# Optimization experiments

Measured on AMD Instinct MI355X. Metric: run time of the kernel, lower is better.

Reference implementation:

```python
import jax, jax.numpy as jnp
import numpy as np

B, N, L, H = 8, 64, 256, 768
E = 2 * H            # 1536, concat(subj, obj)
NH = 12              # attention heads
HD = E // NH         # 128 head dim
HL = 1024            # LSTM hidden
C = 42               # num classes
SCALE = 0.02         # param scale for numerical sanity


def setup_inputs() -> dict:
    key = jax.random.key(0)
    ks = jax.random.split(key, 19)
    rn = lambda k, s: jax.random.normal(k, s, jnp.float32) * SCALE
    return {
        "hidden": jax.random.normal(ks[0], (B, N, L, H), jnp.float32),
        "entity_pair_inds": jax.random.randint(ks[1], (B, N, 2), 0, L),
        "Wkey": jax.random.uniform(ks[2], (E, E), jnp.float32) * SCALE,
        "Wque": jax.random.uniform(ks[3], (E, E), jnp.float32) * SCALE,
        "Wval": jax.random.uniform(ks[4], (E, E), jnp.float32) * SCALE,
        "in_proj_w": rn(ks[5], (3 * E, E)),
        "in_proj_b": rn(ks[6], (3 * E,)),
        "out_proj_w": rn(ks[7], (E, E)),
        "out_proj_b": rn(ks[8], (E,)),
        "Wih_f": rn(ks[9], (4 * HL, E)),
        "Whh_f": rn(ks[10], (4 * HL, HL)),
        "bih_f": rn(ks[11], (4 * HL,)),
        "bhh_f": rn(ks[12], (4 * HL,)),
        "Wih_b": rn(ks[13], (4 * HL, E)),
        "Whh_b": rn(ks[14], (4 * HL, HL)),
        "bih_b": rn(ks[15], (4 * HL,)),
        "bhh_b": rn(ks[16], (4 * HL,)),
        "out_w": rn(ks[17], (C, 2 * HL)),
        "out_b": rn(ks[18], (C,)),
    }


def _mha(q_in, k_in, v_in, in_proj_w, in_proj_b, out_proj_w, out_proj_b):
    # torch nn.MultiheadAttention, batch_first
    Wq, Wk, Wv = jnp.split(in_proj_w, 3, axis=0)
    bq, bk, bv = jnp.split(in_proj_b, 3, axis=0)
    b, n, _ = q_in.shape
    q = (q_in @ Wq.T + bq).reshape(b, n, NH, HD)
    k = (k_in @ Wk.T + bk).reshape(b, n, NH, HD)
    v = (v_in @ Wv.T + bv).reshape(b, n, NH, HD)
    scores = jnp.einsum("bnhd,bmhd->bhnm", q, k) / np.sqrt(HD).astype(np.float32)
    attn = jax.nn.softmax(scores, axis=-1)
    o = jnp.einsum("bhnm,bmhd->bnhd", attn, v).reshape(b, n, E)
    return o @ out_proj_w.T + out_proj_b


def _lstm_dir(x, Wih, Whh, bih, bhh):
    # single-direction LSTM over an unbatched sequence x: (T, E)
    def step(carry, xt):
        h, c = carry
        g = xt @ Wih.T + bih + h @ Whh.T + bhh  # (4*HL,)
        i, f, gg, o = jnp.split(g, 4)
        i, f, o = jax.nn.sigmoid(i), jax.nn.sigmoid(f), jax.nn.sigmoid(o)
        c = f * c + i * jnp.tanh(gg)
        h = o * jnp.tanh(c)
        return (h, c), h
    init = (jnp.zeros(HL, x.dtype), jnp.zeros(HL, x.dtype))
    _, hs = jax.lax.scan(step, init, x)
    return hs  # (T, HL)


def reference(hidden, entity_pair_inds, Wkey, Wque, Wval, in_proj_w, in_proj_b,
              out_proj_w, out_proj_b, Wih_f, Whh_f, bih_f, bhh_f,
              Wih_b, Whh_b, bih_b, bhh_b, out_w, out_b):
    # vectorized entity-pair gather: (B, N, 2) indices into token axis L
    idx = entity_pair_inds[:, :, :, None]                      # (B,N,2,1)
    pair = jnp.take_along_axis(hidden, idx, axis=2)            # (B,N,2,H)
    cat = pair.reshape(B, N, 2 * H)                            # (B,N,1536) = [subj; obj]
    keys = cat @ Wkey
    queries = cat @ Wque
    values = cat @ Wval
    # original calls attn(keys, queries, values) -> query=keys, key=queries, value=values
    attn_out = _mha(keys, queries, values, in_proj_w, in_proj_b, out_proj_w, out_proj_b)
    avg = jnp.sum(attn_out * cat, axis=1) / N                  # (B, E)
    # dropout is identity in eval mode
    # torch LSTM treats 2D input as unbatched sequence of length B
    hf = _lstm_dir(avg, Wih_f, Whh_f, bih_f, bhh_f)            # (B, HL)
    hb = _lstm_dir(avg[::-1], Wih_b, Whh_b, bih_b, bhh_b)[::-1]
    lstm_out = jnp.concatenate([hf, hb], axis=-1)              # (B, 2*HL)
    logits = lstm_out @ out_w.T + out_b                        # (B, C)
    return jax.nn.softmax(logits, axis=1)
```

## Files before the change

### kernel.cpp

```cpp
#include <hip/hip_runtime.h>
#include <hip/hip_bf16.h>
#include <cstdint>


typedef __attribute__((ext_vector_type(8))) short short8_t;
typedef __attribute__((ext_vector_type(4))) float f32x4_t;

__device__ __forceinline__ uint4 pack8(float4 a, float4 b) {
  union { uint4 u; __hip_bfloat16 h[8]; } pk;
  pk.h[0] = __float2bfloat16(a.x); pk.h[1] = __float2bfloat16(a.y);
  pk.h[2] = __float2bfloat16(a.z); pk.h[3] = __float2bfloat16(a.w);
  pk.h[4] = __float2bfloat16(b.x); pk.h[5] = __float2bfloat16(b.y);
  pk.h[6] = __float2bfloat16(b.z); pk.h[7] = __float2bfloat16(b.w);
  return pk.u;
}

__global__ __launch_bounds__(256) void prep_all_kernel(
    const float* __restrict__ hidden, const int* __restrict__ inds,
    const float* __restrict__ Wkey, const float* __restrict__ Wque, const float* __restrict__ Wval,
    float* __restrict__ cat, __hip_bfloat16* __restrict__ cat16,
    __hip_bfloat16* __restrict__ Wt16, float* __restrict__ avg0) {
  const int bid = blockIdx.x, tid = threadIdx.x;
  if (bid < 512) {
    if (bid < 48) avg0[bid * 256 + tid] = 0.f;
    int bn = bid;
    int i0 = inds[bn * 2 + 0], i1 = inds[bn * 2 + 1];
    const float* r0 = hidden + ((size_t)bn * 256 + i0) * 768;
    const float* r1 = hidden + ((size_t)bn * 256 + i1) * 768;
    float* c = cat + (size_t)bn * 1536;
    __hip_bfloat16* c16 = cat16 + (size_t)bn * 1536;
    for (int i = tid; i < 768; i += 256) {
      float a = r0[i], b = r1[i];
      c[i] = a; c[768 + i] = b;
      c16[i] = __float2bfloat16(a); c16[768 + i] = __float2bfloat16(b);
    }
  } else {
    int b2 = bid - 512;
    int z = b2 / 576, rem = b2 % 576, by = rem / 24, bx = rem % 24;
    const float* W = z == 0 ? Wkey : (z == 1 ? Wque : Wval);
    __hip_bfloat16* O = Wt16 + (size_t)z * 1536 * 1536;
    __shared__ float tile[64][65];
    int n0 = bx * 64, k0 = by * 64;
    int r = tid >> 2, q = tid & 3;
#pragma unroll
    for (int j = 0; j < 4; ++j) {
      float4 v = *(const float4*)(W + (size_t)(k0 + r) * 1536 + n0 + q * 16 + j * 4);
      tile[r][q * 16 + j * 4 + 0] = v.x; tile[r][q * 16 + j * 4 + 1] = v.y;
      tile[r][q * 16 + j * 4 + 2] = v.z; tile[r][q * 16 + j * 4 + 3] = v.w;
    }
    __syncthreads();
    union { uint4 u[2]; __hip_bfloat16 h[16]; } pk;
#pragma unroll
    for (int i = 0; i < 16; ++i) pk.h[i] = __float2bfloat16(tile[q * 16 + i][r]);
    __hip_bfloat16* dst = O + (size_t)(n0 + r) * 1536 + k0 + q * 16;
    *(uint4*)dst = pk.u[0];
    *(uint4*)(dst + 8) = pk.u[1];
  }
}

template <int CMODE, bool BIAS, int TAIL>
__global__ __launch_bounds__(256) void mfma_gemm(
    const __hip_bfloat16* __restrict__ A, long As,
    const __hip_bfloat16* __restrict__ Bm, long Bs,
    const float* __restrict__ bias, long biasS,
    void* __restrict__ Cp, long Cs,
    const float* __restrict__ catp, float* __restrict__ avgp,
    const float* __restrict__ tail_src_f, const float* __restrict__ tail_src_b,
    __hip_bfloat16* __restrict__ tail_dst) {
  constexpr int K = 1536, N = 1536;
  const int bid = blockIdx.x, t = threadIdx.x;
  if (TAIL == 1 && bid >= 1152) {
    int tb = bid - 1152;
#pragma unroll
    for (int c = 0; c < 4; ++c) {
      int i = tb * 1024 + c * 256 + t;
      float4 a = ((const float4*)tail_src_f)[2 * i], b = ((const float4*)tail_src_f)[2 * i + 1];
      *(uint4*)(tail_dst + (size_t)i * 8) = pack8(a, b);
    }
    return;
  }
  if (TAIL == 2 && bid >= 1152) {
    int tb = bid - 1152;
#pragma unroll
    for (int c = 0; c < 4; ++c) {
      int id = tb * 1024 + c * 256 + t;
      int lane = id & 63, half = (id >> 6) & 1, row = (id >> 7) & 4095, d = id >> 19;
      const float* W = d ? tail_src_b : tail_src_f;
      const float* srcp = W + (size_t)row * 1024 + half * 512 + lane;
      union { uint4 u; __hip_bfloat16 h[8]; } pk;
#pragma unroll
      for (int e = 0; e < 8; ++e) pk.h[e] = __float2bfloat16(srcp[e * 64]);
      *(uint4*)(tail_dst + (size_t)id * 8) = pk.u;
    }
    return;
  }
  const int L = bid % 384, z = bid / 384;
  A += (size_t)z * As; Bm += (size_t)z * Bs;
  if (BIAS) bias += (size_t)z * biasS;
  __shared__ __align__(16) short Abuf[32 * 64];
  __shared__ __align__(16) short Bbuf[64 * 64];
  const int bxs = (L & 7) + 8 * ((L >> 3) % 3);
  const int bys = (L >> 3) / 3;
  const int i0 = bys * 32, j0 = bxs * 64;
  const int lane = t & 63, wave = t >> 6;
  f32x4_t acc[2] = {};

  const int rA = t >> 3, qA = t & 7;
  const char* Ag = (const char*)(A + (size_t)(i0 + rA) * K) + qA * 16;
  char* const Asw = (char*)Abuf + ((rA * 128 + qA * 16) ^ ((rA & 7) << 4));
  const int rB0 = t >> 3, qB0 = t & 7;
  const int tb1 = t + 256, rB1 = tb1 >> 3, qB1 = tb1 & 7;
  const char* Bg0 = (const char*)(Bm + (size_t)(j0 + rB0) * K) + qB0 * 16;
  const char* Bg1 = (const char*)(Bm + (size_t)(j0 + rB1) * K) + qB1 * 16;
  char* const Bsw0 = (char*)Bbuf + ((rB0 * 128 + qB0 * 16) ^ ((rB0 & 7) << 4));
  char* const Bsw1 = (char*)Bbuf + ((rB1 * 128 + qB1 * 16) ^ ((rB1 & 7) << 4));

  for (int kb = 0; kb < K * 2; kb += 128) {
    uint4 a0 = *(const uint4*)(Ag + kb);
    uint4 b0 = *(const uint4*)(Bg0 + kb);
    uint4 b1 = *(const uint4*)(Bg1 + kb);
    __syncthreads();
    *(uint4*)Asw = a0;
    *(uint4*)Bsw0 = b0; *(uint4*)Bsw1 = b1;
    __syncthreads();
#pragma unroll
    for (int ks = 0; ks < 2; ++ks) {
      short8_t af[2], bf;
#pragma unroll
      for (int mi = 0; mi < 2; ++mi) {
        int rr = mi * 16 + (lane & 15);
        int off = (rr * 128 + ks * 64 + (lane >> 4) * 16) ^ ((rr & 7) << 4);
        af[mi] = *(const short8_t*)((const char*)Abuf + off);
      }
      {
        int rr = wave * 16 + (lane & 15);
        int off = (rr * 128 + ks * 64 + (lane >> 4) * 16) ^ ((rr & 7) << 4);
        bf = *(const short8_t*)((const char*)Bbuf + off);
      }
#pragma unroll
      for (int mi = 0; mi < 2; ++mi)
        acc[mi] = __builtin_amdgcn_mfma_f32_16x16x32_bf16(af[mi], bf, acc[mi], 0, 0, 0);
    }
  }
  const int col = j0 + wave * 16 + (lane & 15);
  if (CMODE == 2) {
    const int b = bys >> 1;
    float bv = bias[col];
    float p = 0.f;
#pragma unroll
    for (int mi = 0; mi < 2; ++mi) {
      int rbase = i0 + mi * 16 + (lane >> 4) * 4;
#pragma unroll
      for (int r = 0; r < 4; ++r)
        p += (acc[mi][r] + bv) * catp[(size_t)(rbase + r) * 1536 + col];
    }
    p += __shfl_xor(p, 16);
    p += __shfl_xor(p, 32);
    if (lane < 16) atomicAdd(&avgp[(size_t)b * 1536 + col], p * (1.0f / 64.0f));
  } else {
    float bv = BIAS ? bias[col] : 0.f;
#pragma unroll
    for (int mi = 0; mi < 2; ++mi) {
      int r0 = i0 + mi * 16 + (lane >> 4) * 4;
#pragma unroll
      for (int r = 0; r < 4; ++r) {
        float val = acc[mi][r] + bv;
        if (CMODE == 1)
          ((__hip_bfloat16*)Cp)[(size_t)z * Cs + (size_t)(r0 + r) * N + col] = __float2bfloat16(val);
        else
          ((float*)Cp)[(size_t)z * Cs + (size_t)(r0 + r) * N + col] = val;
      }
    }
  }
}

__global__ __launch_bounds__(256) void attn2_kernel(
    const __hip_bfloat16* __restrict__ qkv, __hip_bfloat16* __restrict__ o,
    const float* __restrict__ opw, __hip_bfloat16* __restrict__ outproj16) {
  __shared__ __align__(16) ushort Qs[64 * 128];
  __shared__ __align__(16) ushort Ks[64 * 128];
  __shared__ __align__(16) ushort Vt[128 * 72];
  __shared__ __align__(16) ushort Ps[64 * 72];
  __shared__ float redmax[2][64];
  __shared__ float redsum[2][64];
  const int tid = threadIdx.x;
  if (blockIdx.x >= 96) {
    int tb = blockIdx.x - 96;
#pragma unroll
    for (int c = 0; c < 4; ++c) {
      int i = tb * 1024 + c * 256 + tid;
      float4 a = ((const float4*)opw)[2 * i], b = ((const float4*)opw)[2 * i + 1];
      *(uint4*)(outproj16 + (size_t)i * 8) = pack8(a, b);
    }
    return;
  }
  const int b = blockIdx.x / 12, h = blockIdx.x % 12;
  const int lane = tid & 63, wave = tid >> 6;
  const int wr = wave >> 1, wc = wave & 1;
  const size_t base = (size_t)b * 64 * 1536 + (size_t)h * 128;
  const __hip_bfloat16* qg = qkv + base;
  const __hip_bfloat16* kg = qkv + 786432 + base;
  const __hip_bfloat16* vg = qkv + 2 * 786432 + base;

  for (int s = tid; s < 1024; s += 256) {
    int row = s >> 4, q4 = s & 15;
    int q4s = (q4 & 8) | ((q4 & 7) ^ (row & 7));
    uint4 qv = *(const uint4*)(qg + (size_t)row * 1536 + q4 * 8);
    uint4 kv = *(const uint4*)(kg + (size_t)row * 1536 + q4 * 8);
    *(uint4*)&Qs[row * 128 + q4s * 8] = qv;
    *(uint4*)&Ks[row * 128 + q4s * 8] = kv;
    uint4 vv = *(const uint4*)(vg + (size_t)row * 1536 + q4 * 8);
    const ushort* ve = (const ushort*)&vv;
    int colv = (((row >> 3) ^ (q4 & 7)) << 3) | (row & 7);
#pragma unroll
    for (int e = 0; e < 8; ++e) Vt[(q4 * 8 + e) * 72 + colv] = ve[e];
  }
  __syncthreads();

  f32x4_t sacc[2][2] = {};
#pragma unroll
  for (int ks = 0; ks < 4; ++ks) {
    short8_t qf[2], kf[2];
#pragma unroll
    for (int mi = 0; mi < 2; ++mi) {
      int rr = wr * 32 + mi * 16 + (lane & 15);
      int slot = ks * 4 + (lane >> 4);
      int slot2 = (slot & 8) | ((slot & 7) ^ (rr & 7));
      qf[mi] = *(const short8_t*)&Qs[rr * 128 + slot2 * 8];
    }
#pragma unroll
    for (int ni = 0; ni < 2; ++ni) {
      int rr = wc * 32 + ni * 16 + (lane & 15);
      int slot = ks * 4 + (lane >> 4);
      int slot2 = (slot & 8) | ((slot & 7) ^ (rr & 7));
      kf[ni] = *(const short8_t*)&Ks[rr * 128 + slot2 * 8];
    }
#pragma unroll
    for (int mi = 0; mi < 2; ++mi)
#pragma unroll
      for (int ni = 0; ni < 2; ++ni)
        sacc[mi][ni] = __builtin_amdgcn_mfma_f32_16x16x32_bf16(qf[mi], kf[ni], sacc[mi][ni], 0, 0, 0);
  }

  const float scale = 0.08838834764831845f;
  float pv[2][2][4];
#pragma unroll
  for (int mi = 0; mi < 2; ++mi)
#pragma unroll
    for (int r = 0; r < 4; ++r) {
      float a0 = sacc[mi][0][r] * scale, a1 = sacc[mi][1][r] * scale;
      pv[mi][0][r] = a0; pv[mi][1][r] = a1;
      float m0 = fmaxf(a0, a1);
      m0 = fmaxf(m0, __shfl_xor(m0, 1));
      m0 = fmaxf(m0, __shfl_xor(m0, 2));
      m0 = fmaxf(m0, __shfl_xor(m0, 4));
      m0 = fmaxf(m0, __shfl_xor(m0, 8));
      if ((lane & 15) == 0) redmax[wc][wr * 32 + mi * 16 + (lane >> 4) * 4 + r] = m0;
    }
  __syncthreads();
#pragma unroll
  for (int mi = 0; mi < 2; ++mi)
#pragma unroll
    for (int r = 0; r < 4; ++r) {
      int row = wr * 32 + mi * 16 + (lane >> 4) * 4 + r;
      float gm = fmaxf(redmax[0][row], redmax[1][row]);
      float e0 = __expf(pv[mi][0][r] - gm);
      float e1 = __expf(pv[mi][1][r] - gm);
      pv[mi][0][r] = e0; pv[mi][1][r] = e1;
      float s0 = e0 + e1;
      s0 += __shfl_xor(s0, 1);
      s0 += __shfl_xor(s0, 2);
      s0 += __shfl_xor(s0, 4);
      s0 += __shfl_xor(s0, 8);
      if ((lane & 15) == 0) redsum[wc][row] = s0;
      int col0 = wc * 32 + (lane & 15);
      Ps[row * 72 + col0] = __bfloat16_as_ushort(__float2bfloat16(e0));
      Ps[row * 72 + col0 + 16] = __bfloat16_as_ushort(__float2bfloat16(e1));
    }
  __syncthreads();

  f32x4_t oacc[2][4] = {};
#pragma unroll
  for (int ks = 0; ks < 2; ++ks) {
    short8_t pf[2], vf[4];
#pragma unroll
    for (int mi = 0; mi < 2; ++mi) {
      int rr = wr * 32 + mi * 16 + (lane & 15);
      pf[mi] = *(const short8_t*)&Ps[rr * 72 + ks * 32 + (lane >> 4) * 8];
    }
#pragma unroll
    for (int ni = 0; ni < 4; ++ni) {
      int rr = wc * 64 + ni * 16 + (lane & 15);
      int mb = (ks * 4 + (lane >> 4)) ^ ((rr >> 3) & 7);
      vf[ni] = *(const short8_t*)&Vt[rr * 72 + mb * 8];
    }
#pragma unroll
    for (int mi = 0; mi < 2; ++mi)
#pragma unroll
      for (int ni = 0; ni < 4; ++ni)
        oacc[mi][ni] = __builtin_amdgcn_mfma_f32_16x16x32_bf16(pf[mi], vf[ni], oacc[mi][ni], 0, 0, 0);
  }

#pragma unroll
  for (int mi = 0; mi < 2; ++mi)
#pragma unroll
    for (int r = 0; r < 4; ++r) {
      int row = wr * 32 + mi * 16 + (lane >> 4) * 4 + r;
      float inv = 1.f / (redsum[0][row] + redsum[1][row]);
#pragma unroll
      for (int ni = 0; ni < 4; ++ni) {
        int col = wc * 64 + ni * 16 + (lane & 15);
        o[base + (size_t)row * 1536 + col] = __float2bfloat16(oacc[mi][ni][r] * inv);
      }
    }
}

__global__ __launch_bounds__(256) void lstm_pre3_kernel(
    const float* __restrict__ avg,
    const float* __restrict__ Wih_f, const float* __restrict__ bih_f, const float* __restrict__ bhh_f,
    const float* __restrict__ Wih_b, const float* __restrict__ bih_b, const float* __restrict__ bhh_b,
    float* __restrict__ xg, float* __restrict__ hstate, float* __restrict__ cstate,
    float* __restrict__ hout) {
  __shared__ float g4[4];
  const int bid = blockIdx.x, tid = threadIdx.x;
  const int wave = tid >> 6, lane = tid & 63;
  const int d = bid >> 10, u = bid & 1023;
  const int j = wave * 1024 + u;
  const float* W = d ? Wih_b : Wih_f;
  const float4* wrow = (const float4*)(W + (size_t)j * 1536);
  float4 w[6];
#pragma unroll
  for (int c = 0; c < 6; ++c) w[c] = wrow[c * 64 + lane];
  float s[8] = {};
#pragma unroll
  for (int r = 0; r < 8; ++r) {
    const float4* av = (const float4*)(avg + (size_t)r * 1536);
#pragma unroll
    for (int c = 0; c < 6; ++c) {
      float4 x = av[c * 64 + lane];
      s[r] += w[c].x * x.x + w[c].y * x.y + w[c].z * x.z + w[c].w * x.w;
    }
  }
#pragma unroll
  for (int r = 0; r < 8; ++r)
#pragma unroll
    for (int off = 32; off; off >>= 1) s[r] += __shfl_xor(s[r], off);
  const int r0 = d ? 7 : 0;
  if (lane == 0) {
    float bias = d ? (bih_b[j] + bhh_b[j]) : (bih_f[j] + bhh_f[j]);
#pragma unroll
    for (int r = 0; r < 8; ++r) xg[((size_t)d * 8 + r) * 4096 + j] = s[r] + bias;
    g4[wave] = s[r0] + bias;
  }
  __syncthreads();
  if (tid == 0) {
    float iv = 1.f / (1.f + __expf(-g4[0]));
    float ov = 1.f / (1.f + __expf(-g4[3]));
    float cn = iv * tanhf(g4[2]);
    float hn = ov * tanhf(cn);
    cstate[(size_t)d * 1024 + u] = cn;
    hstate[(size_t)(2 + d) * 1024 + u] = hn;
    hout[((size_t)d * 8 + r0) * 1024 + u] = hn;
  }
}

__global__ __launch_bounds__(256) void lstm_step2_kernel(
    const __hip_bfloat16* __restrict__ whh16s, const float* __restrict__ xg,
    float* __restrict__ hstate, float* __restrict__ cstate,
    float* __restrict__ hout, int s) {
  const int bid = blockIdx.x;
  const int d = bid >> 8, u0 = (bid & 255) * 4;
  const int tid = threadIdx.x, wave = tid >> 6, lane = tid & 63;
  const float* hread = hstate + ((size_t)(s & 1) * 2 + d) * 1024;
  float* hwrite = hstate + ((size_t)((s + 1) & 1) * 2 + d) * 1024;
  float* c = cstate + (size_t)d * 1024;
  const int r = d ? (7 - s) : s;

  float hreg[16];
#pragma unroll
  for (int cc = 0; cc < 16; ++cc) hreg[cc] = hread[cc * 64 + lane];

  __shared__ float gsm[4][4];
#pragma unroll
  for (int ui = 0; ui < 4; ++ui) {
    int row = wave * 1024 + u0 + ui;
    const uint4* wp = (const uint4*)whh16s + ((size_t)d * 4096 + row) * 128 + lane;
    uint4 w0 = wp[0];
    uint4 w1 = wp[64];
    float sacc = 0.f;
#pragma unroll
    for (int e4 = 0; e4 < 4; ++e4) {
      uint32_t u = ((const uint32_t*)&w0)[e4];
      sacc += __uint_as_float(u << 16) * hreg[2 * e4] +
              __uint_as_float(u & 0xffff0000u) * hreg[2 * e4 + 1];
    }
#pragma unroll
    for (int e4 = 0; e4 < 4; ++e4) {
      uint32_t u = ((const uint32_t*)&w1)[e4];
      sacc += __uint_as_float(u << 16) * hreg[8 + 2 * e4] +
              __uint_as_float(u & 0xffff0000u) * hreg[8 + 2 * e4 + 1];
    }
#pragma unroll
    for (int off = 32; off; off >>= 1) sacc += __shfl_xor(sacc, off);
    if (lane == 0) gsm[wave][ui] = sacc;
  }
  __syncthreads();
  if (tid < 4) {
    int u = u0 + tid;
    const float* xgr = xg + ((size_t)d * 8 + r) * 4096;
    float gi = gsm[0][tid] + xgr[u];
    float gf = gsm[1][tid] + xgr[1024 + u];
    float gg = gsm[2][tid] + xgr[2048 + u];
    float go = gsm[3][tid] + xgr[3072 + u];
    float iv = 1.f / (1.f + __expf(-gi));
    float fv = 1.f / (1.f + __expf(-gf));
    float ov = 1.f / (1.f + __expf(-go));
    float cold = c[u];
    float cn = fv * cold + iv * tanhf(gg);
    float hn = ov * tanhf(cn);
    c[u] = cn;
    hwrite[u] = hn;
    hout[((size_t)d * 8 + r) * 1024 + u] = hn;
  }
}

__global__ __launch_bounds__(256) void final_kernel(
    const float* __restrict__ hout, const float* __restrict__ out_w,
    const float* __restrict__ out_b, float* __restrict__ outp) {
  __shared__ float lo[2048];
  __shared__ float logits[64];
  const int s = blockIdx.x, tid = threadIdx.x;
  for (int i = tid; i < 1024; i += 256) {
    lo[i] = hout[(size_t)s * 1024 + i];
    lo[1024 + i] = hout[(size_t)(8 + s) * 1024 + i];
  }
  __syncthreads();
  const int wave = tid >> 6, lane = tid & 63;
  for (int cls = wave; cls < 42; cls += 4) {
    const float4* wr = (const float4*)(out_w + (size_t)cls * 2048);
    const float4* xr = (const float4*)lo;
    float acc = 0.f;
#pragma unroll
    for (int t = 0; t < 8; ++t) {
      int k4 = lane + t * 64;
      float4 w = wr[k4];
      float4 x = xr[k4];
      acc += w.x * x.x + w.y * x.y + w.z * x.z + w.w * x.w;
    }
#pragma unroll
    for (int off = 32; off; off >>= 1) acc += __shfl_xor(acc, off);
    if (lane == 0) logits[cls] = acc + out_b[cls];
  }
  __syncthreads();
  if (tid == 0) {
    float mx = -1e30f;
    for (int c2 = 0; c2 < 42; ++c2) mx = fmaxf(mx, logits[c2]);
    float sum = 0.f;
    for (int c2 = 0; c2 < 42; ++c2) {
      float e = __expf(logits[c2] - mx);
      logits[c2] = e;
      sum += e;
    }
    float inv = 1.f / sum;
    for (int c2 = 0; c2 < 42; ++c2) outp[s * 42 + c2] = logits[c2] * inv;
  }
}

extern "C" void kernel_launch(void* const* d_in, const int* in_sizes, int n_in,
                              void* d_out, int out_size, void* d_ws, size_t ws_size,
                              hipStream_t stream) {
  const float* hidden     = (const float*)d_in[0];
  const int*   inds       = (const int*)d_in[1];
  const float* Wkey       = (const float*)d_in[2];
  const float* Wque       = (const float*)d_in[3];
  const float* Wval       = (const float*)d_in[4];
  const float* in_proj_w  = (const float*)d_in[5];
  const float* in_proj_b  = (const float*)d_in[6];
  const float* out_proj_w = (const float*)d_in[7];
  const float* out_proj_b = (const float*)d_in[8];
  const float* Wih_f      = (const float*)d_in[9];
  const float* Whh_f      = (const float*)d_in[10];
  const float* bih_f      = (const float*)d_in[11];
  const float* bhh_f      = (const float*)d_in[12];
  const float* Wih_b      = (const float*)d_in[13];
  const float* Whh_b      = (const float*)d_in[14];
  const float* bih_b      = (const float*)d_in[15];
  const float* bhh_b      = (const float*)d_in[16];
  const float* out_w      = (const float*)d_in[17];
  const float* out_b      = (const float*)d_in[18];
  float* out = (float*)d_out;

  float* ws = (float*)d_ws;
  float* cat      = ws;
  float* avg      = cat + 786432;
  float* xg       = avg + 12288;
  float* hstate   = xg + 65536;
  float* cstate   = hstate + 4096;
  float* hout     = cstate + 2048;
  __hip_bfloat16* b16 = (__hip_bfloat16*)(hout + 16384);
  __hip_bfloat16* cat16     = b16;
  __hip_bfloat16* Wt16      = cat16 + 786432;
  __hip_bfloat16* inproj16  = Wt16 + 7077888;
  __hip_bfloat16* outproj16 = inproj16 + 7077888;
  __hip_bfloat16* kqv1      = outproj16 + 2359296;
  __hip_bfloat16* qkv16     = kqv1 + 2359296;
  __hip_bfloat16* ob16      = qkv16 + 2359296;
  __hip_bfloat16* whh16s    = ob16 + 786432;

  prep_all_kernel<<<2240, 256, 0, stream>>>(hidden, inds, Wkey, Wque, Wval,
                                            cat, cat16, Wt16, avg);

  mfma_gemm<1, false, 1><<<2016, 256, 0, stream>>>(
      cat16, 0, Wt16, 1536L * 1536, nullptr, 0, kqv1, 786432, nullptr, nullptr,
      in_proj_w, nullptr, inproj16);
  mfma_gemm<1, true, 2><<<2176, 256, 0, stream>>>(
      kqv1, 786432, inproj16, 1536L * 1536, in_proj_b, 1536, qkv16, 786432,
      nullptr, nullptr, Whh_f, Whh_b, whh16s);

  attn2_kernel<<<384, 256, 0, stream>>>(qkv16, ob16, out_proj_w, outproj16);

  mfma_gemm<2, true, 0><<<384, 256, 0, stream>>>(
      ob16, 0, outproj16, 0, out_proj_b, 0, nullptr, 0, cat, avg,
      nullptr, nullptr, nullptr);

  lstm_pre3_kernel<<<2048, 256, 0, stream>>>(avg, Wih_f, bih_f, bhh_f, Wih_b, bih_b, bhh_b,
                                             xg, hstate, cstate, hout);

  for (int s = 1; s < 8; ++s)
    lstm_step2_kernel<<<512, 256, 0, stream>>>(whh16s, xg, hstate, cstate, hout, s);

  final_kernel<<<8, 256, 0, stream>>>(hout, out_w, out_b, out);
}
```

Baseline: 145.6 us.

## Fuse LSTM recurrent steps and final classifier into one cooperative persistent kernel

```diff
diff --git a/kernel.cpp b/kernel.cpp
--- a/kernel.cpp
+++ b/kernel.cpp
@@ -320,9 +320,10 @@
     const float* __restrict__ Wih_f, const float* __restrict__ bih_f, const float* __restrict__ bhh_f,
     const float* __restrict__ Wih_b, const float* __restrict__ bih_b, const float* __restrict__ bhh_b,
     float* __restrict__ xg, float* __restrict__ hstate, float* __restrict__ cstate,
-    float* __restrict__ hout) {
+    float* __restrict__ hout, uint32_t* __restrict__ bar) {
   __shared__ float g4[4];
   const int bid = blockIdx.x, tid = threadIdx.x;
+  if (bid == 0 && tid == 0) *bar = 0u;
   const int wave = tid >> 6, lane = tid & 63;
   const int d = bid >> 10, u = bid & 1023;
   const int j = wave * 1024 + u;
@@ -364,105 +365,130 @@
   }
 }
 
-__global__ __launch_bounds__(256) void lstm_step2_kernel(
+__global__ __launch_bounds__(256) void lstm_steps_kernel(
     const __hip_bfloat16* __restrict__ whh16s, const float* __restrict__ xg,
-    float* __restrict__ hstate, float* __restrict__ cstate,
-    float* __restrict__ hout, int s) {
+    float* __restrict__ hstate, const float* __restrict__ cstate,
+    float* __restrict__ hout,
+    const float* __restrict__ out_w, const float* __restrict__ out_b,
+    float* __restrict__ outp, uint32_t* __restrict__ bar) {
+  __shared__ float gsm[4][4];
+  __shared__ float lo[2048];
+  __shared__ float logits[64];
   const int bid = blockIdx.x;
   const int d = bid >> 8, u0 = (bid & 255) * 4;
   const int tid = threadIdx.x, wave = tid >> 6, lane = tid & 63;
-  const float* hread = hstate + ((size_t)(s & 1) * 2 + d) * 1024;
-  float* hwrite = hstate + ((size_t)((s + 1) & 1) * 2 + d) * 1024;
-  float* c = cstate + (size_t)d * 1024;
-  const int r = d ? (7 - s) : s;
-
-  float hreg[16];
-#pragma unroll
-  for (int cc = 0; cc < 16; ++cc) hreg[cc] = hread[cc * 64 + lane];
-
-  __shared__ float gsm[4][4];
-#pragma unroll
-  for (int ui = 0; ui < 4; ++ui) {
-    int row = wave * 1024 + u0 + ui;
-    const uint4* wp = (const uint4*)whh16s + ((size_t)d * 4096 + row) * 128 + lane;
-    uint4 w0 = wp[0];
-    uint4 w1 = wp[64];
-    float sacc = 0.f;
-#pragma unroll
-    for (int e4 = 0; e4 < 4; ++e4) {
-      uint32_t u = ((const uint32_t*)&w0)[e4];
-      sacc += __uint_as_float(u << 16) * hreg[2 * e4] +
-              __uint_as_float(u & 0xffff0000u) * hreg[2 * e4 + 1];
-    }
-#pragma unroll
-    for (int e4 = 0; e4 < 4; ++e4) {
-      uint32_t u = ((const uint32_t*)&w1)[e4];
-      sacc += __uint_as_float(u << 16) * hreg[8 + 2 * e4] +
-              __uint_as_float(u & 0xffff0000u) * hreg[8 + 2 * e4 + 1];
-    }
-#pragma unroll
-    for (int off = 32; off; off >>= 1) sacc += __shfl_xor(sacc, off);
-    if (lane == 0) gsm[wave][ui] = sacc;
+
+  float creg = (tid < 4) ? cstate[(size_t)d * 1024 + u0 + tid] : 0.f;
+  uint32_t phase = 0;
+
+  for (int s = 1; s < 8; ++s) {
+    if (s > 1) {
+      __syncthreads();
+      if (tid == 0) {
+        __threadfence();
+        atomicAdd(bar, 1u);
+        uint32_t target = 512u * (++phase);
+        while (atomicAdd(bar, 0u) < target) __builtin_amdgcn_s_sleep(2);
+        __threadfence();
+      }
+      __syncthreads();
+      if (tid != 0) ++phase;
+    }
+    const float* hread = hstate + ((size_t)(s & 1) * 2 + d) * 1024;
+    float* hwrite = hstate + ((size_t)((s + 1) & 1) * 2 + d) * 1024;
+    const int r = d ? (7 - s) : s;
+
+    float hreg[16];
+#pragma unroll
+    for (int cc = 0; cc < 16; ++cc) hreg[cc] = hread[cc * 64 + lane];
+
+#pragma unroll
+    for (int ui = 0; ui < 4; ++ui) {
+      int row = wave * 1024 + u0 + ui;
+      const uint4* wp = (const uint4*)whh16s + ((size_t)d * 4096 + row) * 128 + lane;
+      uint4 w0 = wp[0];
+      uint4 w1 = wp[64];
+      float sacc = 0.f;
+#pragma unroll
+      for (int e4 = 0; e4 < 4; ++e4) {
+        uint32_t u = ((const uint32_t*)&w0)[e4];
+        sacc += __uint_as_float(u << 16) * hreg[2 * e4] +
+                __uint_as_float(u & 0xffff0000u) * hreg[2 * e4 + 1];
+      }
+#pragma unroll
+      for (int e4 = 0; e4 < 4; ++e4) {
+        uint32_t u = ((const uint32_t*)&w1)[e4];
+        sacc += __uint_as_float(u << 16) * hreg[8 + 2 * e4] +
+                __uint_as_float(u & 0xffff0000u) * hreg[8 + 2 * e4 + 1];
+      }
+#pragma unroll
+      for (int off = 32; off; off >>= 1) sacc += __shfl_xor(sacc, off);
+      if (lane == 0) gsm[wave][ui] = sacc;
+    }
+    __syncthreads();
+    if (tid < 4) {
+      int u = u0 + tid;
+      const float* xgr = xg + ((size_t)d * 8 + r) * 4096;
+      float gi = gsm[0][tid] + xgr[u];
+      float gf = gsm[1][tid] + xgr[1024 + u];
+      float gg = gsm[2][tid] + xgr[2048 + u];
+      float go = gsm[3][tid] + xgr[3072 + u];
+      float iv = 1.f / (1.f + __expf(-gi));
+      float fv = 1.f / (1.f + __expf(-gf));
+      float ov = 1.f / (1.f + __expf(-go));
+      float cn = fv * creg + iv * tanhf(gg);
+      float hn = ov * tanhf(cn);
+      creg = cn;
+      hwrite[u] = hn;
+      hout[((size_t)d * 8 + r) * 1024 + u] = hn;
+    }
+    __syncthreads();
+  }
+
+  if (tid == 0) {
+    __threadfence();
+    atomicAdd(bar, 1u);
+    uint32_t target = 512u * (phase + 1);
+    while (atomicAdd(bar, 0u) < target) __builtin_amdgcn_s_sleep(2);
+    __threadfence();
   }
   __syncthreads();
-  if (tid < 4) {
-    int u = u0 + tid;
-    const float* xgr = xg + ((size_t)d * 8 + r) * 4096;
-    float gi = gsm[0][tid] + xgr[u];
-    float gf = gsm[1][tid] + xgr[1024 + u];
-    float gg = gsm[2][tid] + xgr[2048 + u];
-    float go = gsm[3][tid] + xgr[3072 + u];
-    float iv = 1.f / (1.f + __expf(-gi));
-    float fv = 1.f / (1.f + __expf(-gf));
-    float ov = 1.f / (1.f + __expf(-go));
-    float cold = c[u];
-    float cn = fv * cold + iv * tanhf(gg);
-    float hn = ov * tanhf(cn);
-    c[u] = cn;
-    hwrite[u] = hn;
-    hout[((size_t)d * 8 + r) * 1024 + u] = hn;
-  }
-}
-
-__global__ __launch_bounds__(256) void final_kernel(
-    const float* __restrict__ hout, const float* __restrict__ out_w,
-    const float* __restrict__ out_b, float* __restrict__ outp) {
-  __shared__ float lo[2048];
-  __shared__ float logits[64];
-  const int s = blockIdx.x, tid = threadIdx.x;
-  for (int i = tid; i < 1024; i += 256) {
-    lo[i] = hout[(size_t)s * 1024 + i];
-    lo[1024 + i] = hout[(size_t)(8 + s) * 1024 + i];
-  }
-  __syncthreads();
-  const int wave = tid >> 6, lane = tid & 63;
-  for (int cls = wave; cls < 42; cls += 4) {
-    const float4* wr = (const float4*)(out_w + (size_t)cls * 2048);
-    const float4* xr = (const float4*)lo;
-    float acc = 0.f;
-#pragma unroll
-    for (int t = 0; t < 8; ++t) {
-      int k4 = lane + t * 64;
-      float4 w = wr[k4];
-      float4 x = xr[k4];
-      acc += w.x * x.x + w.y * x.y + w.z * x.z + w.w * x.w;
-    }
-#pragma unroll
-    for (int off = 32; off; off >>= 1) acc += __shfl_xor(acc, off);
-    if (lane == 0) logits[cls] = acc + out_b[cls];
-  }
-  __syncthreads();
-  if (tid == 0) {
-    float mx = -1e30f;
-    for (int c2 = 0; c2 < 42; ++c2) mx = fmaxf(mx, logits[c2]);
-    float sum = 0.f;
-    for (int c2 = 0; c2 < 42; ++c2) {
-      float e = __expf(logits[c2] - mx);
-      logits[c2] = e;
-      sum += e;
-    }
-    float inv = 1.f / sum;
-    for (int c2 = 0; c2 < 42; ++c2) outp[s * 42 + c2] = logits[c2] * inv;
+
+  if (bid < 8) {
+    const int s = bid;
+    for (int i = tid; i < 1024; i += 256) {
+      lo[i] = hout[(size_t)s * 1024 + i];
+      lo[1024 + i] = hout[(size_t)(8 + s) * 1024 + i];
+    }
+    __syncthreads();
+    for (int cls = wave; cls < 42; cls += 4) {
+      const float4* wr2 = (const float4*)(out_w + (size_t)cls * 2048);
+      const float4* xr = (const float4*)lo;
+      float acc = 0.f;
+#pragma unroll
+      for (int t2 = 0; t2 < 8; ++t2) {
+        int k4 = lane + t2 * 64;
+        float4 w = wr2[k4];
+        float4 x = xr[k4];
+        acc += w.x * x.x + w.y * x.y + w.z * x.z + w.w * x.w;
+      }
+#pragma unroll
+      for (int off = 32; off; off >>= 1) acc += __shfl_xor(acc, off);
+      if (lane == 0) logits[cls] = acc + out_b[cls];
+    }
+    __syncthreads();
+    if (tid == 0) {
+      float mx = -1e30f;
+      for (int c2 = 0; c2 < 42; ++c2) mx = fmaxf(mx, logits[c2]);
+      float sum = 0.f;
+      for (int c2 = 0; c2 < 42; ++c2) {
+        float e = __expf(logits[c2] - mx);
+        logits[c2] = e;
+        sum += e;
+      }
+      float inv = 1.f / sum;
+      for (int c2 = 0; c2 < 42; ++c2) outp[s * 42 + c2] = logits[c2] * inv;
+    }
   }
 }
 
@@ -497,7 +523,8 @@
   float* hstate   = xg + 65536;
   float* cstate   = hstate + 4096;
   float* hout     = cstate + 2048;
-  __hip_bfloat16* b16 = (__hip_bfloat16*)(hout + 16384);
+  uint32_t* bar   = (uint32_t*)(hout + 16384);
+  __hip_bfloat16* b16 = (__hip_bfloat16*)(hout + 16384 + 64);
   __hip_bfloat16* cat16     = b16;
   __hip_bfloat16* Wt16      = cat16 + 786432;
   __hip_bfloat16* inproj16  = Wt16 + 7077888;
@@ -524,10 +551,9 @@
       nullptr, nullptr, nullptr);
 
   lstm_pre3_kernel<<<2048, 256, 0, stream>>>(avg, Wih_f, bih_f, bhh_f, Wih_b, bih_b, bhh_b,
-                                             xg, hstate, cstate, hout);
-
-  for (int s = 1; s < 8; ++s)
-    lstm_step2_kernel<<<512, 256, 0, stream>>>(whh16s, xg, hstate, cstate, hout, s);
-
-  final_kernel<<<8, 256, 0, stream>>>(hout, out_w, out_b, out);
-}
+                                             xg, hstate, cstate, hout, bar);
+
+  void* args[] = {(void*)&whh16s, (void*)&xg, (void*)&hstate, (void*)&cstate,
+                  (void*)&hout, (void*)&out_w, (void*)&out_b, (void*)&out, (void*)&bar};
+  hipLaunchCooperativeKernel((void*)lstm_steps_kernel, dim3(512), dim3(256), args, 0, stream);
+}
```

New measurement: 402.7 us. 177% more time.
